# Kernel tuning notes

Measured on AMD Instinct MI355X. Metric: run time of the kernel, lower is better.

Reference implementation:

```python
import jax, jax.numpy as jnp
import numpy as np

N_NODES = 8192
N_EDGES = 262144
D_IN = 512
D_OUT = 512


def setup_inputs() -> dict:
    key = jax.random.key(0)
    k1, k2, k3 = jax.random.split(key, 3)
    x = jax.random.normal(k1, (N_NODES, D_IN), dtype=jnp.float32)
    edge_index = jax.random.randint(k2, (2, N_EDGES), 0, N_NODES, dtype=jnp.int64)
    weight = jax.random.normal(k3, (D_IN, D_OUT), dtype=jnp.float32)
    bias = jnp.zeros((D_OUT,), dtype=jnp.float32)
    return {"x": x, "edge_index": edge_index, "weight": weight, "bias": bias}


def reference(x, edge_index, weight, bias):
    # GCN layer with selfloop=True branch of the original module.
    n = x.shape[0]
    # Dense symmetric adjacency via scatter-set, matching adj[ei0,ei1]=1; adj[ei1,ei0]=1
    adj = jnp.zeros((n, n), dtype=x.dtype)
    adj = adj.at[edge_index[0], edge_index[1]].set(1.0)
    adj = adj.at[edge_index[1], edge_index[0]].set(1.0)
    # Add self loops, symmetric degree normalization D^{-1/2} A D^{-1/2}
    adj = adj + jnp.eye(n, dtype=x.dtype)
    deg = jnp.sum(adj, axis=1)
    dinv = 1.0 / jnp.sqrt(deg)
    adj = adj * dinv[:, None] * dinv[None, :]  # == D @ adj @ D (diagonal scaling)
    return adj @ (x @ weight) + bias
```

## Files before the change

### kernel.cpp

```cpp
#include <hip/hip_runtime.h>
#include <hip/hip_bf16.h>


#define ELL_STRIDE 128

typedef __attribute__((ext_vector_type(8))) short bf16x8;
typedef __attribute__((ext_vector_type(4))) float f32x4;
typedef __attribute__((ext_vector_type(2))) float f32x2;

__device__ __forceinline__ unsigned short f2bf(float f) {
  unsigned u = __float_as_uint(f);
  u = (u + 0x7fff + ((u >> 16) & 1)) >> 16;
  return (unsigned short)u;
}
__device__ __forceinline__ float bflo(unsigned u) {
  return __uint_as_float(u << 16);
}
__device__ __forceinline__ float bfhi(unsigned u) {
  return __uint_as_float(u & 0xffff0000u);
}

__global__ __launch_bounds__(256) void fused_front_kernel(
    const int* __restrict__ ei, unsigned* __restrict__ mask, int n_edges,
    int words,
    const float* __restrict__ x, unsigned short* __restrict__ xb, int n4,
    const float* __restrict__ W, unsigned short* __restrict__ Wt, int K, int N,
    unsigned short* __restrict__ Hs, float* __restrict__ dinv, int n_nodes,
    int edge_blocks, int cast_blocks, int tr_blocks) {
  const int bid = blockIdx.x;
  if (bid < edge_blocks) {
    const int e = bid * 256 + threadIdx.x;
    if (e < n_edges) {
      const int u = ei[e];
      const int v = ei[e + n_edges];
      atomicOr(&mask[(size_t)u * words + (v >> 5)], 1u << (v & 31));
      atomicOr(&mask[(size_t)v * words + (u >> 5)], 1u << (u & 31));
    }
    return;
  }
  if (bid < edge_blocks + cast_blocks) {
    const int t = (bid - edge_blocks) * 256 + threadIdx.x;
    if (t < n4) {
      float4 v = ((const float4*)x)[t];
      ushort4 o;
      o.x = f2bf(v.x); o.y = f2bf(v.y); o.z = f2bf(v.z); o.w = f2bf(v.w);
      ((ushort4*)xb)[t] = o;
    }
    return;
  }
  if (bid < edge_blocks + cast_blocks + tr_blocks) {
    __shared__ float tile[32][33];
    const int b = bid - edge_blocks - cast_blocks;
    const int bx = b & ((N >> 5) - 1);
    const int by = b >> (31 - __builtin_clz(N >> 5));
    const int tx = threadIdx.x & 31;
    const int ty = threadIdx.x >> 5;
#pragma unroll
    for (int r = 0; r < 4; ++r)
      tile[ty + 8 * r][tx] = W[(size_t)(by * 32 + ty + 8 * r) * N + bx * 32 + tx];
    __syncthreads();
#pragma unroll
    for (int r = 0; r < 4; ++r)
      Wt[(size_t)(bx * 32 + ty + 8 * r) * K + by * 32 + tx] =
          f2bf(tile[tx][ty + 8 * r]);
    return;
  }
  {
    const int t = threadIdx.x;
    if (t < (N >> 1)) ((unsigned*)(Hs + (size_t)n_nodes * N))[t] = 0;
    if (t == 0) dinv[n_nodes] = 0.f;
  }
}

__global__ __launch_bounds__(256) void fused_mid_kernel(
    const unsigned short* __restrict__ xb,
    const unsigned short* __restrict__ Wt,
    unsigned short* __restrict__ Hs,
    const unsigned* __restrict__ mask, unsigned short* __restrict__ ell,
    int* __restrict__ deg, float* __restrict__ dinv,
    int M, int N, int K, int words, int gemm_blocks, int nbx_sh) {
  __shared__ unsigned short As[512 * 8];
  __shared__ unsigned short Bs[1024 * 8];

  const int tid = threadIdx.x;
  const int bid = blockIdx.x;

  if (bid < gemm_blocks) {
    const int wave = tid >> 6;
    const int lane = tid & 63;
    const int q = lane >> 4;
    const int c = lane & 15;
    const int bx = bid & ((1 << nbx_sh) - 1);
    const int by = bid >> nbx_sh;
    const int m0 = by * 64;
    const int n0 = bx * 128;
    const int wr = wave >> 1, wc = wave & 1;

    f32x4 acc[2][4] = {};

    for (int k0 = 0; k0 < K; k0 += 64) {
#pragma unroll
      for (int t = 0; t < 2; ++t) {
        const int sbase = t * 256 + wave * 64;
        const int s = sbase + lane;
        const unsigned short* g =
            xb + (size_t)(m0 + (s & 63)) * K + k0 + (s >> 6) * 8;
        __builtin_amdgcn_global_load_lds(
            (const __attribute__((address_space(1))) void*)g,
            (__attribute__((address_space(3))) void*)(As + sbase * 8), 16, 0, 0);
      }
#pragma unroll
      for (int t = 0; t < 4; ++t) {
        const int sbase = t * 256 + wave * 64;
        const int s = sbase + lane;
        const int bn = s >> 3;
        const int bk = (s & 7) ^ (bn & 7);
        const unsigned short* g =
            Wt + (size_t)(n0 + bn) * K + k0 + bk * 8;
        __builtin_amdgcn_global_load_lds(
            (const __attribute__((address_space(1))) void*)g,
            (__attribute__((address_space(3))) void*)(Bs + sbase * 8), 16, 0, 0);
      }
      __syncthreads();

#pragma unroll
      for (int kk = 0; kk < 2; ++kk) {
        bf16x8 a[2], b[4];
#pragma unroll
        for (int tm = 0; tm < 2; ++tm) {
          const int row = wr * 32 + tm * 16 + c;
          a[tm] = *(const bf16x8*)(As + (((kk * 4 + q) * 64) + row) * 8);
        }
#pragma unroll
        for (int tn = 0; tn < 4; ++tn) {
          const int n = wc * 64 + tn * 16 + c;
          b[tn] = *(const bf16x8*)(Bs + (n * 8 + ((kk * 4 + q) ^ (n & 7))) * 8);
        }
#pragma unroll
        for (int tm = 0; tm < 2; ++tm)
#pragma unroll
          for (int tn = 0; tn < 4; ++tn)
            acc[tm][tn] = __builtin_amdgcn_mfma_f32_16x16x32_bf16(
                a[tm], b[tn], acc[tm][tn], 0, 0, 0);
      }
      __syncthreads();
    }

#pragma unroll
    for (int tm = 0; tm < 2; ++tm) {
#pragma unroll
      for (int r = 0; r < 4; ++r) {
        const int grow = m0 + wr * 32 + tm * 16 + q * 4 + r;
#pragma unroll
        for (int tn = 0; tn < 4; ++tn) {
          const int gcol = n0 + wc * 64 + tn * 16 + c;
          Hs[(size_t)grow * N + gcol] = f2bf(acc[tm][tn][r]);
        }
      }
    }
    return;
  }

  {
    const int wave = tid >> 6, lane = tid & 63;
    const int node = (bid - gemm_blocks) * 4 + wave;
    const unsigned* __restrict__ row = mask + (size_t)node * words;
    unsigned short* __restrict__ out = ell + (size_t)node * ELL_STRIDE;

    int running = 0;
    for (int r = 0; r < words; r += 64) {
      const int w = r + lane;
      unsigned bits = row[w];
      const int cnt = __popc(bits);
      int x = cnt;
#pragma unroll
      for (int d = 1; d < 64; d <<= 1) {
        int y = __shfl_up(x, d, 64);
        if (lane >= d) x += y;
      }
      int pos = running + x - cnt;
      while (bits) {
        const int b = __builtin_ctz(bits);
        bits &= bits - 1;
        if (pos < ELL_STRIDE) out[pos] = (unsigned short)((w << 5) + b);
        ++pos;
      }
      running += __shfl(x, 63, 64);
    }
    for (int p = running + lane; p < ELL_STRIDE; p += 64)
      out[p] = (unsigned short)(p == running ? node : M);
    if (lane == 0) {
      const int dd = running + 1;
      deg[node] = dd < ELL_STRIDE ? dd : ELL_STRIDE;
      dinv[node] = rsqrtf((float)running + 1.0f);
    }
  }
}

__global__ __launch_bounds__(1024) void spmm_kernel(
    const unsigned short* __restrict__ ell, const int* __restrict__ deg,
    const float* __restrict__ dinv, const unsigned short* __restrict__ Hs,
    const float* __restrict__ bias, float* __restrict__ out, int n, int D) {
  __shared__ float sdinv[8193];
  __shared__ uint2 ji[16][ELL_STRIDE];
  const int tid = threadIdx.x;
  const int wave = tid >> 6, lane = tid & 63;
  const int bid = blockIdx.x;
  const int qt = bid & 3;
  const int i = (bid >> 2) * 16 + wave;
  const unsigned rowbytes = (unsigned)(D * 2);

  for (int t = tid; t < n + 1; t += 1024) sdinv[t] = dinv[t];
  __syncthreads();

  {
    const unsigned j0 = ell[(size_t)i * ELL_STRIDE + lane];
    const unsigned j1 = ell[(size_t)i * ELL_STRIDE + 64 + lane];
    ji[wave][lane] = make_uint2(j0 * rowbytes, __float_as_uint(sdinv[j0]));
    ji[wave][64 + lane] = make_uint2(j1 * rowbytes, __float_as_uint(sdinv[j1]));
  }
  const int d = deg[i];
  const float di = sdinv[i];
  const int kmax = (d + 7) & ~7;

  const char* __restrict__ hb = (const char*)Hs + qt * 256 + lane * 4;
  float a0 = 0.f, a1 = 0.f;

#pragma unroll 8
  for (int k = 0; k < kmax; ++k) {
    const uint2 e = ji[wave][k];
    const float dj = __uint_as_float(e.y);
    const unsigned hv = *(const unsigned*)(hb + e.x);
    a0 += dj * bflo(hv);
    a1 += dj * bfhi(hv);
  }

  const int col = qt * (D >> 2) + lane * 2;
  const float2 b = *(const float2*)(bias + col);
  f32x2 o;
  o.x = di * a0 + b.x;
  o.y = di * a1 + b.y;
  __builtin_nontemporal_store(o, (f32x2*)(out + (size_t)i * D + col));
}

extern "C" void kernel_launch(void* const* d_in, const int* in_sizes, int n_in,
                              void* d_out, int out_size, void* d_ws, size_t ws_size,
                              hipStream_t stream) {
  const float* x    = (const float*)d_in[0];
  const int*   ei   = (const int*)d_in[1];
  const float* W    = (const float*)d_in[2];
  const float* bias = (const float*)d_in[3];
  float* out = (float*)d_out;

  const int d_out_dim = in_sizes[3];
  const int d_in_dim  = in_sizes[2] / d_out_dim;
  const int n_nodes   = in_sizes[0] / d_in_dim;
  const int n_edges   = in_sizes[1] / 2;
  const int words     = (n_nodes + 31) / 32;

  char* ws = (char*)d_ws;
  size_t off = 0;
  unsigned* mask = (unsigned*)(ws + off); off += (size_t)n_nodes * words * 4;
  int* deg       = (int*)(ws + off);      off += (size_t)n_nodes * 4;
  float* dinv    = (float*)(ws + off);    off += (size_t)(n_nodes + 1) * 4;
  unsigned short* ell = (unsigned short*)(ws + off); off += (size_t)n_nodes * ELL_STRIDE * 2;
  unsigned short* xb  = (unsigned short*)(ws + off); off += (size_t)n_nodes * d_in_dim * 2;
  unsigned short* Wt  = (unsigned short*)(ws + off); off += (size_t)d_in_dim * d_out_dim * 2;
  unsigned short* Hs  = (unsigned short*)(ws + off);
  off += (size_t)(n_nodes + 1) * d_out_dim * 2;

  hipMemsetAsync(mask, 0, (size_t)n_nodes * words * 4, stream);

  const int edge_blocks = (n_edges + 255) / 256;
  const int n4 = n_nodes * d_in_dim / 4;
  const int cast_blocks = (n4 + 255) / 256;
  const int tr_blocks = (d_in_dim / 32) * (d_out_dim / 32);
  fused_front_kernel<<<edge_blocks + cast_blocks + tr_blocks + 1, 256, 0, stream>>>(
      ei, mask, n_edges, words, x, xb, n4, W, Wt, d_in_dim, d_out_dim,
      Hs, dinv, n_nodes, edge_blocks, cast_blocks, tr_blocks);

  const int nbx = d_out_dim / 128;
  const int nbx_sh = 31 - __builtin_clz(nbx);
  const int gemm_blocks = nbx * (n_nodes / 64);
  const int ell_blocks = n_nodes / 4;
  fused_mid_kernel<<<gemm_blocks + ell_blocks, 256, 0, stream>>>(
      xb, Wt, Hs, mask, ell, deg, dinv,
      n_nodes, d_out_dim, d_in_dim, words, gemm_blocks, nbx_sh);

  const int spmm_blocks = 4 * (n_nodes / 16);
  spmm_kernel<<<spmm_blocks, 1024, 0, stream>>>(ell, deg, dinv, Hs, bias, out,
                                                n_nodes, d_out_dim);
}
```

Measured before the change: 150.7 us.

## Fold column degree scaling into GEMM epilogue and slim SpMM

A separate degree kernel now counts mask bits per row and writes dinv before the GEMM runs. The GEMM epilogue multiplies each output row of H by dinv, so the SpMM no longer needs per-neighbor scale factors. This removes the 33KB shared-memory copy of dinv that every SpMM block made and the per-edge multiply. The SpMM now runs 256-thread blocks with a smaller index table. The cost is an extra kernel launch plus a second pass over the mask, and each output row is now rounded to bf16 after scaling.

```diff
diff --git a/kernel.cpp b/kernel.cpp
--- a/kernel.cpp
+++ b/kernel.cpp
@@ -25,7 +25,7 @@
     int words,
     const float* __restrict__ x, unsigned short* __restrict__ xb, int n4,
     const float* __restrict__ W, unsigned short* __restrict__ Wt, int K, int N,
-    unsigned short* __restrict__ Hs, float* __restrict__ dinv, int n_nodes,
+    unsigned short* __restrict__ Hs, int n_nodes,
     int edge_blocks, int cast_blocks, int tr_blocks) {
   const int bid = blockIdx.x;
   if (bid < edge_blocks) {
@@ -68,8 +68,19 @@
   {
     const int t = threadIdx.x;
     if (t < (N >> 1)) ((unsigned*)(Hs + (size_t)n_nodes * N))[t] = 0;
-    if (t == 0) dinv[n_nodes] = 0.f;
-  }
+  }
+}
+
+__global__ __launch_bounds__(256) void deg_kernel(
+    const unsigned* __restrict__ mask, float* __restrict__ dinv, int words) {
+  const int wave = threadIdx.x >> 6, lane = threadIdx.x & 63;
+  const int node = blockIdx.x * 4 + wave;
+  const unsigned* __restrict__ row = mask + (size_t)node * words;
+  int cnt = 0;
+  for (int w = lane; w < words; w += 64) cnt += __popc(row[w]);
+#pragma unroll
+  for (int d = 1; d < 64; d <<= 1) cnt += __shfl_xor(cnt, d, 64);
+  if (lane == 0) dinv[node] = rsqrtf((float)cnt + 1.0f);
 }
 
 __global__ __launch_bounds__(256) void fused_mid_kernel(
@@ -77,7 +88,7 @@
     const unsigned short* __restrict__ Wt,
     unsigned short* __restrict__ Hs,
     const unsigned* __restrict__ mask, unsigned short* __restrict__ ell,
-    int* __restrict__ deg, float* __restrict__ dinv,
+    int* __restrict__ deg, const float* __restrict__ dinv,
     int M, int N, int K, int words, int gemm_blocks, int nbx_sh) {
   __shared__ unsigned short As[512 * 8];
   __shared__ unsigned short Bs[1024 * 8];
@@ -151,10 +162,11 @@
 #pragma unroll
       for (int r = 0; r < 4; ++r) {
         const int grow = m0 + wr * 32 + tm * 16 + q * 4 + r;
+        const float dr = dinv[grow];
 #pragma unroll
         for (int tn = 0; tn < 4; ++tn) {
           const int gcol = n0 + wc * 64 + tn * 16 + c;
-          Hs[(size_t)grow * N + gcol] = f2bf(acc[tm][tn][r]);
+          Hs[(size_t)grow * N + gcol] = f2bf(dr * acc[tm][tn][r]);
         }
       }
     }
@@ -192,35 +204,29 @@
     if (lane == 0) {
       const int dd = running + 1;
       deg[node] = dd < ELL_STRIDE ? dd : ELL_STRIDE;
-      dinv[node] = rsqrtf((float)running + 1.0f);
-    }
-  }
-}
-
-__global__ __launch_bounds__(1024) void spmm_kernel(
+    }
+  }
+}
+
+__global__ __launch_bounds__(256) void spmm_kernel(
     const unsigned short* __restrict__ ell, const int* __restrict__ deg,
     const float* __restrict__ dinv, const unsigned short* __restrict__ Hs,
     const float* __restrict__ bias, float* __restrict__ out, int n, int D) {
-  __shared__ float sdinv[8193];
-  __shared__ uint2 ji[16][ELL_STRIDE];
-  const int tid = threadIdx.x;
-  const int wave = tid >> 6, lane = tid & 63;
+  __shared__ unsigned ji[4][ELL_STRIDE];
+  const int wave = threadIdx.x >> 6, lane = threadIdx.x & 63;
   const int bid = blockIdx.x;
   const int qt = bid & 3;
-  const int i = (bid >> 2) * 16 + wave;
+  const int i = (bid >> 2) * 4 + wave;
   const unsigned rowbytes = (unsigned)(D * 2);
-
-  for (int t = tid; t < n + 1; t += 1024) sdinv[t] = dinv[t];
-  __syncthreads();
 
   {
     const unsigned j0 = ell[(size_t)i * ELL_STRIDE + lane];
     const unsigned j1 = ell[(size_t)i * ELL_STRIDE + 64 + lane];
-    ji[wave][lane] = make_uint2(j0 * rowbytes, __float_as_uint(sdinv[j0]));
-    ji[wave][64 + lane] = make_uint2(j1 * rowbytes, __float_as_uint(sdinv[j1]));
+    ji[wave][lane] = j0 * rowbytes;
+    ji[wave][64 + lane] = j1 * rowbytes;
   }
   const int d = deg[i];
-  const float di = sdinv[i];
+  const float di = dinv[i];
   const int kmax = (d + 7) & ~7;
 
   const char* __restrict__ hb = (const char*)Hs + qt * 256 + lane * 4;
@@ -228,11 +234,10 @@
 
 #pragma unroll 8
   for (int k = 0; k < kmax; ++k) {
-    const uint2 e = ji[wave][k];
-    const float dj = __uint_as_float(e.y);
-    const unsigned hv = *(const unsigned*)(hb + e.x);
-    a0 += dj * bflo(hv);
-    a1 += dj * bfhi(hv);
+    const unsigned off = ji[wave][k];
+    const unsigned hv = *(const unsigned*)(hb + off);
+    a0 += bflo(hv);
+    a1 += bfhi(hv);
   }
 
   const int col = qt * (D >> 2) + lane * 2;
@@ -277,7 +282,9 @@
   const int tr_blocks = (d_in_dim / 32) * (d_out_dim / 32);
   fused_front_kernel<<<edge_blocks + cast_blocks + tr_blocks + 1, 256, 0, stream>>>(
       ei, mask, n_edges, words, x, xb, n4, W, Wt, d_in_dim, d_out_dim,
-      Hs, dinv, n_nodes, edge_blocks, cast_blocks, tr_blocks);
+      Hs, n_nodes, edge_blocks, cast_blocks, tr_blocks);
+
+  deg_kernel<<<n_nodes / 4, 256, 0, stream>>>(mask, dinv, words);
 
   const int nbx = d_out_dim / 128;
   const int nbx_sh = 31 - __builtin_clz(nbx);
@@ -287,7 +294,7 @@
       xb, Wt, Hs, mask, ell, deg, dinv,
       n_nodes, d_out_dim, d_in_dim, words, gemm_blocks, nbx_sh);
 
-  const int spmm_blocks = 4 * (n_nodes / 16);
-  spmm_kernel<<<spmm_blocks, 1024, 0, stream>>>(ell, deg, dinv, Hs, bias, out,
-                                                n_nodes, d_out_dim);
-}
+  const int spmm_blocks = 4 * (n_nodes / 4);
+  spmm_kernel<<<spmm_blocks, 256, 0, stream>>>(ell, deg, dinv, Hs, bias, out,
+                                               n_nodes, d_out_dim);
+}
```

New measurement: 151.5 us. About the same (+0.6%).

## Fold mask memset into prep kernel and overlap edge scatter with GEMM

Applied to the files above, without the earlier changes.

Replaces the separate hipMemsetAsync of the adjacency bitmask with zeroing blocks inside the prep kernel (alongside cast and transpose). The edge atomicOr scatter moves into the same launch as the GEMM so the two overlap, and the ELL construction becomes its own kernel after that launch. This removes one memset launch and hides scatter latency under GEMM work, at the cost of an extra kernel launch for ELL building.

```diff
diff --git a/kernel.cpp b/kernel.cpp
--- a/kernel.cpp
+++ b/kernel.cpp
@@ -20,26 +20,26 @@
   return __uint_as_float(u & 0xffff0000u);
 }
 
-__global__ __launch_bounds__(256) void fused_front_kernel(
-    const int* __restrict__ ei, unsigned* __restrict__ mask, int n_edges,
-    int words,
+__global__ __launch_bounds__(256) void prep_kernel(
+    unsigned* __restrict__ mask, int mask_words_total,
     const float* __restrict__ x, unsigned short* __restrict__ xb, int n4,
     const float* __restrict__ W, unsigned short* __restrict__ Wt, int K, int N,
     unsigned short* __restrict__ Hs, float* __restrict__ dinv, int n_nodes,
-    int edge_blocks, int cast_blocks, int tr_blocks) {
+    int mset_blocks, int cast_blocks, int tr_blocks) {
   const int bid = blockIdx.x;
-  if (bid < edge_blocks) {
-    const int e = bid * 256 + threadIdx.x;
-    if (e < n_edges) {
-      const int u = ei[e];
-      const int v = ei[e + n_edges];
-      atomicOr(&mask[(size_t)u * words + (v >> 5)], 1u << (v & 31));
-      atomicOr(&mask[(size_t)v * words + (u >> 5)], 1u << (u & 31));
+  if (bid < mset_blocks) {
+    uint4* m4 = (uint4*)mask;
+    const int n16 = mask_words_total >> 2;
+    const uint4 z = make_uint4(0u, 0u, 0u, 0u);
+#pragma unroll
+    for (int r = 0; r < 4; ++r) {
+      const int t = (bid * 4 + r) * 256 + threadIdx.x;
+      if (t < n16) m4[t] = z;
     }
     return;
   }
-  if (bid < edge_blocks + cast_blocks) {
-    const int t = (bid - edge_blocks) * 256 + threadIdx.x;
+  if (bid < mset_blocks + cast_blocks) {
+    const int t = (bid - mset_blocks) * 256 + threadIdx.x;
     if (t < n4) {
       float4 v = ((const float4*)x)[t];
       ushort4 o;
@@ -48,9 +48,9 @@
     }
     return;
   }
-  if (bid < edge_blocks + cast_blocks + tr_blocks) {
+  if (bid < mset_blocks + cast_blocks + tr_blocks) {
     __shared__ float tile[32][33];
-    const int b = bid - edge_blocks - cast_blocks;
+    const int b = bid - mset_blocks - cast_blocks;
     const int bx = b & ((N >> 5) - 1);
     const int by = b >> (31 - __builtin_clz(N >> 5));
     const int tx = threadIdx.x & 31;
@@ -72,12 +72,11 @@
   }
 }
 
-__global__ __launch_bounds__(256) void fused_mid_kernel(
+__global__ __launch_bounds__(256) void front2_kernel(
     const unsigned short* __restrict__ xb,
     const unsigned short* __restrict__ Wt,
     unsigned short* __restrict__ Hs,
-    const unsigned* __restrict__ mask, unsigned short* __restrict__ ell,
-    int* __restrict__ deg, float* __restrict__ dinv,
+    const int* __restrict__ ei, unsigned* __restrict__ mask, int n_edges,
     int M, int N, int K, int words, int gemm_blocks, int nbx_sh) {
   __shared__ unsigned short As[512 * 8];
   __shared__ unsigned short Bs[1024 * 8];
@@ -162,38 +161,50 @@
   }
 
   {
-    const int wave = tid >> 6, lane = tid & 63;
-    const int node = (bid - gemm_blocks) * 4 + wave;
-    const unsigned* __restrict__ row = mask + (size_t)node * words;
-    unsigned short* __restrict__ out = ell + (size_t)node * ELL_STRIDE;
-
-    int running = 0;
-    for (int r = 0; r < words; r += 64) {
-      const int w = r + lane;
-      unsigned bits = row[w];
-      const int cnt = __popc(bits);
-      int x = cnt;
-#pragma unroll
-      for (int d = 1; d < 64; d <<= 1) {
-        int y = __shfl_up(x, d, 64);
-        if (lane >= d) x += y;
-      }
-      int pos = running + x - cnt;
-      while (bits) {
-        const int b = __builtin_ctz(bits);
-        bits &= bits - 1;
-        if (pos < ELL_STRIDE) out[pos] = (unsigned short)((w << 5) + b);
-        ++pos;
-      }
-      running += __shfl(x, 63, 64);
-    }
-    for (int p = running + lane; p < ELL_STRIDE; p += 64)
-      out[p] = (unsigned short)(p == running ? node : M);
-    if (lane == 0) {
-      const int dd = running + 1;
-      deg[node] = dd < ELL_STRIDE ? dd : ELL_STRIDE;
-      dinv[node] = rsqrtf((float)running + 1.0f);
-    }
+    const int e = (bid - gemm_blocks) * 256 + tid;
+    if (e < n_edges) {
+      const int u = ei[e];
+      const int v = ei[e + n_edges];
+      atomicOr(&mask[(size_t)u * words + (v >> 5)], 1u << (v & 31));
+      atomicOr(&mask[(size_t)v * words + (u >> 5)], 1u << (u & 31));
+    }
+  }
+}
+
+__global__ __launch_bounds__(256) void ell_kernel(
+    const unsigned* __restrict__ mask, unsigned short* __restrict__ ell,
+    int* __restrict__ deg, float* __restrict__ dinv, int M, int words) {
+  const int wave = threadIdx.x >> 6, lane = threadIdx.x & 63;
+  const int node = blockIdx.x * 4 + wave;
+  const unsigned* __restrict__ row = mask + (size_t)node * words;
+  unsigned short* __restrict__ out = ell + (size_t)node * ELL_STRIDE;
+
+  int running = 0;
+  for (int r = 0; r < words; r += 64) {
+    const int w = r + lane;
+    unsigned bits = row[w];
+    const int cnt = __popc(bits);
+    int x = cnt;
+#pragma unroll
+    for (int d = 1; d < 64; d <<= 1) {
+      int y = __shfl_up(x, d, 64);
+      if (lane >= d) x += y;
+    }
+    int pos = running + x - cnt;
+    while (bits) {
+      const int b = __builtin_ctz(bits);
+      bits &= bits - 1;
+      if (pos < ELL_STRIDE) out[pos] = (unsigned short)((w << 5) + b);
+      ++pos;
+    }
+    running += __shfl(x, 63, 64);
+  }
+  for (int p = running + lane; p < ELL_STRIDE; p += 64)
+    out[p] = (unsigned short)(p == running ? node : M);
+  if (lane == 0) {
+    const int dd = running + 1;
+    deg[node] = dd < ELL_STRIDE ? dd : ELL_STRIDE;
+    dinv[node] = rsqrtf((float)running + 1.0f);
   }
 }
 
@@ -269,23 +280,25 @@
   unsigned short* Hs  = (unsigned short*)(ws + off);
   off += (size_t)(n_nodes + 1) * d_out_dim * 2;
 
-  hipMemsetAsync(mask, 0, (size_t)n_nodes * words * 4, stream);
-
-  const int edge_blocks = (n_edges + 255) / 256;
+  const int mask_words_total = n_nodes * words;
+  const int mset_blocks = (mask_words_total / 4 + 1023) / 1024;
   const int n4 = n_nodes * d_in_dim / 4;
   const int cast_blocks = (n4 + 255) / 256;
   const int tr_blocks = (d_in_dim / 32) * (d_out_dim / 32);
-  fused_front_kernel<<<edge_blocks + cast_blocks + tr_blocks + 1, 256, 0, stream>>>(
-      ei, mask, n_edges, words, x, xb, n4, W, Wt, d_in_dim, d_out_dim,
-      Hs, dinv, n_nodes, edge_blocks, cast_blocks, tr_blocks);
+  prep_kernel<<<mset_blocks + cast_blocks + tr_blocks + 1, 256, 0, stream>>>(
+      mask, mask_words_total, x, xb, n4, W, Wt, d_in_dim, d_out_dim,
+      Hs, dinv, n_nodes, mset_blocks, cast_blocks, tr_blocks);
 
   const int nbx = d_out_dim / 128;
   const int nbx_sh = 31 - __builtin_clz(nbx);
   const int gemm_blocks = nbx * (n_nodes / 64);
-  const int ell_blocks = n_nodes / 4;
-  fused_mid_kernel<<<gemm_blocks + ell_blocks, 256, 0, stream>>>(
-      xb, Wt, Hs, mask, ell, deg, dinv,
+  const int edge_blocks = (n_edges + 255) / 256;
+  front2_kernel<<<gemm_blocks + edge_blocks, 256, 0, stream>>>(
+      xb, Wt, Hs, ei, mask, n_edges,
       n_nodes, d_out_dim, d_in_dim, words, gemm_blocks, nbx_sh);
+
+  ell_kernel<<<n_nodes / 4, 256, 0, stream>>>(mask, ell, deg, dinv,
+                                              n_nodes, words);
 
   const int spmm_blocks = 4 * (n_nodes / 16);
   spmm_kernel<<<spmm_blocks, 1024, 0, stream>>>(ell, deg, dinv, Hs, bias, out,
```

After: 147.0 us. 2.5% less time.
